# Kernel tuning notes

Measured on AMD Instinct MI355X. Metric: run time of the kernel, lower is better.

The kernel has to match this reference:

```python
import jax, jax.numpy as jnp
import numpy as np

B, S, D, H = 1, 2048, 1024, 16
HD = D // H  # head_dim = 64


def _split_heads(x):
    # [B,S,D] -> [B,H,S,HD]
    return x.reshape(B, S, H, HD).transpose(0, 2, 1, 3)


def setup_inputs() -> dict:
    key = jax.random.key(0)
    ks = jax.random.split(key, 8)
    p = 0.02
    return {
        "hidden_states": jax.random.normal(ks[0], (B, S, D), jnp.float32),
        "knowledge": jax.random.normal(ks[1], (B, S, D), jnp.float32),
        "Wq": jax.random.normal(ks[2], (2 * D, D), jnp.float32) * p,
        "Wk_know": jax.random.normal(ks[3], (D, D), jnp.float32) * p,
        "Wk_mlp": jax.random.normal(ks[4], (D, D), jnp.float32) * p,
        "Wv_know": jax.random.normal(ks[5], (D, D), jnp.float32) * p,
        "Wv_mlp": jax.random.normal(ks[6], (D, D), jnp.float32) * p,
        "Wo": jax.random.normal(ks[7], (D, D), jnp.float32) * p,
    }


def reference(hidden_states, knowledge, Wq, Wk_know, Wk_mlp, Wv_know, Wv_mlp, Wo):
    shared = jnp.concatenate([hidden_states, knowledge], axis=-1)  # [B,S,2D]
    q = _split_heads(shared @ Wq)            # [B,H,S,HD]
    k_know = _split_heads(knowledge @ Wk_know)
    k_mlp = _split_heads(hidden_states @ Wk_mlp)
    v_know = _split_heads(knowledge @ Wv_know)
    v_mlp = _split_heads(hidden_states @ Wv_mlp)

    scale = jnp.asarray(D, jnp.float32) ** 0.5  # note: full embed_dim, not head_dim
    mask_value = jnp.finfo(jnp.float32).min
    causal = jnp.tril(jnp.ones((S, S), dtype=bool))  # [S,S]

    s_know = jnp.einsum("bhqd,bhkd->bhqk", q, k_know) / scale
    s_know = jnp.where(causal, s_know, mask_value)
    s_mlp = jnp.einsum("bhqd,bhkd->bhqk", q, k_mlp) / scale
    s_mlp = jnp.where(causal, s_mlp, mask_value)

    concat_scores = jax.nn.softmax(jnp.concatenate([s_know, s_mlp], axis=-1), axis=-1)  # [B,H,S,2S]
    concat_values = jnp.concatenate([v_know, v_mlp], axis=-2)  # [B,H,2S,HD]
    out = jnp.einsum("bhqk,bhkd->bhqd", concat_scores, concat_values)
    out = out.transpose(0, 2, 1, 3).reshape(B, S, D) @ Wo  # merge heads + proj_o
    return out, concat_scores
```

## Files before the change

kernel.cpp:

```cpp
#include <hip/hip_runtime.h>

typedef unsigned short u16;
typedef float f32x4 __attribute__((ext_vector_type(4)));
typedef __bf16 bf16x8 __attribute__((ext_vector_type(8)));
typedef unsigned int u32x4 __attribute__((ext_vector_type(4)));
typedef u16 u16x4 __attribute__((ext_vector_type(4)));

#define S_ 2048
#define D_ 1024
#define H_ 16
#define HD_ 64

#define WAITV(N) asm volatile("s_waitcnt vmcnt(" #N ")" ::: "memory")
#define BAR() __builtin_amdgcn_s_barrier()
#define SFENCE() __builtin_amdgcn_sched_barrier(0)

__device__ __forceinline__ u16 f2bf(float f) {
  unsigned int u = __builtin_bit_cast(unsigned int, f);
  u += 0x7fffu + ((u >> 16) & 1u);
  return (u16)(u >> 16);
}

__device__ __forceinline__ f32x4 mfma16(bf16x8 a, bf16x8 b, f32x4 c) {
  return __builtin_amdgcn_mfma_f32_16x16x32_bf16(a, b, c, 0, 0, 0);
}

__device__ __forceinline__ float ex2(float x) {
  float r;
  asm("v_exp_f32 %0, %1\n\ts_nop 1" : "=v"(r) : "v"(x));
  return r;
}

__device__ __forceinline__ void gld_lds16(const u16* g, u16* l) {
  __builtin_amdgcn_global_load_lds((const __attribute__((address_space(1))) void*)g,
                                   (__attribute__((address_space(3))) void*)l, 16, 0, 0);
}

__global__ __launch_bounds__(256) void prep_kernel(
    const float* __restrict__ hs, const float* __restrict__ kn, const float* __restrict__ Wq,
    const float* __restrict__ Wkk, const float* __restrict__ Wvk, const float* __restrict__ Wkm,
    const float* __restrict__ Wvm, const float* __restrict__ Wo, u16* __restrict__ hs_bf,
    u16* __restrict__ kn_bf, u16* __restrict__ WqT, u16* __restrict__ WkvkT,
    u16* __restrict__ WkvmT, u16* __restrict__ WoT, int n4) {
  __shared__ float tile[32][33];
  int b = blockIdx.x;
  if (b < 4096) {
    int i = b * 256 + threadIdx.x;
    const float* s;
    u16* d;
    int j;
    if (i < n4) { s = hs; d = hs_bf; j = i; }
    else { j = i - n4; if (j >= n4) return; s = kn; d = kn_bf; }
    f32x4 v = *(const f32x4*)(s + (size_t)j * 4);
    u16x4 o;
    o[0] = f2bf(v[0]); o[1] = f2bf(v[1]); o[2] = f2bf(v[2]); o[3] = f2bf(v[3]);
    *(u16x4*)(d + (size_t)j * 4) = o;
    return;
  }
  int idx = b - 4096;
  int bc = idx & 31, y = idx >> 5;
  const float* W;
  u16* WT;
  int R, br;
  const size_t HM = (size_t)1024 * 1024;
  if (y < 64) { W = Wq; WT = WqT; R = 2048; br = y; }
  else {
    R = 1024; br = y & 31;
    switch ((y - 64) >> 5) {
      case 0: W = Wkk; WT = WkvkT; break;
      case 1: W = Wvk; WT = WkvkT + HM; break;
      case 2: W = Wkm; WT = WkvmT; break;
      case 3: W = Wvm; WT = WkvmT + HM; break;
      default: W = Wo; WT = WoT; break;
    }
  }
  int tx = threadIdx.x & 31, ty = threadIdx.x >> 5;
#pragma unroll
  for (int i = 0; i < 4; ++i)
    tile[ty + i * 8][tx] = W[(size_t)(br * 32 + ty + i * 8) * 1024 + bc * 32 + tx];
  __syncthreads();
#pragma unroll
  for (int i = 0; i < 4; ++i)
    WT[(size_t)(bc * 32 + ty + i * 8) * R + br * 32 + tx] = f2bf(tile[tx][ty + i * 8]);
}

template <int MODE, int MI, int NI>
__device__ __forceinline__ void gemm_body(u16* smem, const u16* A0, const u16* A1, int ksplit,
                                          const u16* BT, void* Cp, int K, int ldc, int bn,
                                          int bm) {
  constexpr int BM = MI * 32, BN = NI * 32;
  u16* const As0 = smem;
  u16* const Bs0 = smem + 2 * BM * 32;
  const int tid = threadIdx.x, l = tid & 63, w = tid >> 6;
  const int wm = w >> 1, wn = w & 1;
  f32x4 zf = {0.f, 0.f, 0.f, 0.f};
  f32x4 acc[MI][NI];
#pragma unroll
  for (int mi = 0; mi < MI; ++mi)
#pragma unroll
    for (int ni = 0; ni < NI; ++ni) acc[mi][ni] = zf;

  auto STAGE = [&](int b, int t) {
    int k0 = t * 32;
#pragma unroll
    for (int i = 0; i < MI / 2; ++i) {
      int idx = tid + i * 256, r = idx >> 2, c = idx & 3;
      int sc = c ^ ((r >> 1) & 3);
      int k = k0 + sc * 8;
      const u16* src = (k < ksplit) ? (A0 + (size_t)(bm * BM + r) * D_ + k)
                                    : (A1 + (size_t)(bm * BM + r) * D_ + (k - ksplit));
      gld_lds16(src, As0 + b * BM * 32 + idx * 8);
    }
#pragma unroll
    for (int i = 0; i < NI / 2; ++i) {
      int idx = tid + i * 256, r = idx >> 2, c = idx & 3;
      int sc = c ^ ((r >> 1) & 3);
      gld_lds16(BT + (size_t)(bn * BN + r) * K + k0 + sc * 8, Bs0 + b * BN * 32 + idx * 8);
    }
  };

  const int nt = K >> 5;
  STAGE(0, 0);
  int cur = 0;
  for (int t = 0; t < nt; ++t) {
    if (t + 1 < nt) {
      STAGE(cur ^ 1, t + 1);
      if constexpr (MI + NI == 8) { WAITV(4); } else { WAITV(3); }
    } else {
      WAITV(0);
    }
    BAR(); SFENCE();
    const u16* Asc = As0 + cur * BM * 32;
    const u16* Bsc = Bs0 + cur * BN * 32;
    bf16x8 af[MI], bfr[NI];
#pragma unroll
    for (int mi = 0; mi < MI; ++mi) {
      int row = wm * (MI * 16) + mi * 16 + (l & 15);
      int slot = (l >> 4) ^ ((row >> 1) & 3);
      af[mi] = __builtin_bit_cast(bf16x8, *(const u32x4*)(Asc + row * 32 + slot * 8));
    }
#pragma unroll
    for (int ni = 0; ni < NI; ++ni) {
      int row = wn * (NI * 16) + ni * 16 + (l & 15);
      int slot = (l >> 4) ^ ((row >> 1) & 3);
      bfr[ni] = __builtin_bit_cast(bf16x8, *(const u32x4*)(Bsc + row * 32 + slot * 8));
    }
#pragma unroll
    for (int mi = 0; mi < MI; ++mi)
#pragma unroll
      for (int ni = 0; ni < NI; ++ni) acc[mi][ni] = mfma16(af[mi], bfr[ni], acc[mi][ni]);
    SFENCE(); BAR();
    cur ^= 1;
  }

  if constexpr (MODE == 2) {
#pragma unroll
    for (int mi = 0; mi < MI; ++mi)
#pragma unroll
      for (int ni = 0; ni < NI; ++ni) {
        u16x4 pk;
#pragma unroll
        for (int r = 0; r < 4; ++r) pk[r] = f2bf(acc[mi][ni][r]);
        int n = bn * BN + wn * (NI * 16) + ni * 16 + (l & 15);
        int m0 = bm * BM + wm * (MI * 16) + mi * 16 + (l >> 4) * 4;
        *(u16x4*)((u16*)Cp + (size_t)n * S_ + m0) = pk;
      }
  } else if constexpr (MODE == 0) {
    __syncthreads();
    u16* Cs = smem;
#pragma unroll
    for (int mi = 0; mi < MI; ++mi)
#pragma unroll
      for (int ni = 0; ni < NI; ++ni)
#pragma unroll
        for (int r = 0; r < 4; ++r) {
          int row = wm * (MI * 16) + mi * 16 + (l >> 4) * 4 + r;
          int col = wn * (NI * 16) + ni * 16 + (l & 15);
          Cs[row * 144 + col] = f2bf(acc[mi][ni][r]);
        }
    __syncthreads();
    constexpr int CPR = BN / 8;
#pragma unroll
    for (int i = 0; i < BM * CPR / 256; ++i) {
      int idx = tid + i * 256;
      int lr = idx / CPR, cc = idx % CPR;
      u32x4 v = *(const u32x4*)(Cs + lr * 144 + cc * 8);
      *(u32x4*)((u16*)Cp + (size_t)(bm * BM + lr) * ldc + bn * BN + cc * 8) = v;
    }
  } else {
    __syncthreads();
    float* Cs = (float*)smem;
#pragma unroll
    for (int mi = 0; mi < MI; ++mi)
#pragma unroll
      for (int ni = 0; ni < NI; ++ni)
#pragma unroll
        for (int r = 0; r < 4; ++r) {
          int row = wm * (MI * 16) + mi * 16 + (l >> 4) * 4 + r;
          int col = wn * (NI * 16) + ni * 16 + (l & 15);
          Cs[row * 136 + col] = acc[mi][ni][r];
        }
    __syncthreads();
    constexpr int CPR = BN / 4;
#pragma unroll
    for (int i = 0; i < BM * CPR / 256; ++i) {
      int idx = tid + i * 256;
      int lr = idx / CPR, cc = idx % CPR;
      f32x4 v = *(const f32x4*)(Cs + lr * 136 + cc * 4);
      __builtin_nontemporal_store(v, (f32x4*)((float*)Cp + (size_t)(bm * BM + lr) * ldc +
                                              bn * BN + cc * 4));
    }
  }
}

__global__ __launch_bounds__(256) void proj_gemm(const u16* __restrict__ hs_bf,
                                                 const u16* __restrict__ kn_bf,
                                                 const u16* __restrict__ WqT,
                                                 const u16* __restrict__ WkvkT,
                                                 const u16* __restrict__ WkvmT,
                                                 u16* __restrict__ qb, u16* __restrict__ kk,
                                                 u16* __restrict__ km, u16* __restrict__ vkT,
                                                 u16* __restrict__ vmT) {
  __shared__ __attribute__((aligned(16))) u16 smem[18432];
  int bid = blockIdx.x;
  int xcd = bid & 7, ixd = bid >> 3;
  int bm, bn;
  if (ixd < 16) {
    bm = xcd * 2 + (ixd >> 3);
    bn = ixd & 7;
  } else if (ixd >= 64 && ixd < 80) {
    return;
  } else {
    int s = (ixd < 64) ? (ixd - 16) : (48 + (ixd - 80));
    bm = xcd * 2 + (s >> 5);
    bn = 8 + (s & 31);
  }
  const size_t HM = (size_t)1024 * 1024;
  const int BIG = 1 << 30;
  if (bn < 8) {
    gemm_body<0, 4, 4>(smem, hs_bf, kn_bf, 1024, WqT, qb, 2048, 1024, bn, bm);
  } else if (bn < 16) {
    gemm_body<0, 4, 4>(smem, kn_bf, kn_bf, BIG, WkvkT, kk, 1024, 1024, bn - 8, bm);
  } else if (bn < 24) {
    gemm_body<2, 4, 4>(smem, kn_bf, kn_bf, BIG, WkvkT + HM, vkT, 1024, 0, bn - 16, bm);
  } else if (bn < 32) {
    gemm_body<0, 4, 4>(smem, hs_bf, hs_bf, BIG, WkvmT, km, 1024, 1024, bn - 24, bm);
  } else {
    gemm_body<2, 4, 4>(smem, hs_bf, hs_bf, BIG, WkvmT + HM, vmT, 1024, 0, bn - 32, bm);
  }
}

__global__ __launch_bounds__(256) void out_gemm(const u16* __restrict__ aob,
                                                const u16* __restrict__ WoT,
                                                float* __restrict__ out) {
  __shared__ __attribute__((aligned(16))) u16 smem[17408];
  int bid = blockIdx.x;
  int xcd = bid & 7, i = bid >> 3;
  int bm = xcd * 4 + (i >> 3), bn = i & 7;
  gemm_body<1, 2, 4>(smem, aob, aob, 1 << 30, WoT, out, 1024, 1024, bn, bm);
}

__device__ __forceinline__ void stage_async64_t512(u16* dst, const u16* src, int stride,
                                                   int tid) {
  int ci = tid;
  int r = ci >> 3, c = ci & 7;
  int sc = c ^ (r & 7);
  gld_lds16(src + (size_t)r * stride + sc * 8, dst + ci * 8);
}

__device__ __forceinline__ bf16x8 ld_frag64(const u16* lds, int rowbase, int chunkbase, int l) {
  int row = rowbase + (l & 15);
  int chunk = chunkbase + (l >> 4);
  int slot = chunk ^ (row & 7);
  return __builtin_bit_cast(bf16x8, *(const u32x4*)(lds + row * 64 + slot * 8));
}

__global__ __launch_bounds__(512) void attn_kernel(const u16* __restrict__ qb,
                                                   const u16* __restrict__ kk,
                                                   const u16* __restrict__ km,
                                                   const u16* __restrict__ vkT,
                                                   const u16* __restrict__ vmT,
                                                   float* __restrict__ scores,
                                                   u16* __restrict__ ao) {
  const int fid = blockIdx.x;
  const int xcd = fid & 7, ixd = fid >> 3;
  const int h = xcd * 2 + (ixd >> 5);
  const int j = ixd & 31;
  const int a = j >> 1;
  const int qt = (((j & 1) ^ (ixd >> 5)) == 0) ? (31 - a) : a;
  const int tid = threadIdx.x, w = tid >> 6, l = tid & 63;
  const int wk = w & 3, kh = w >> 2;
  const int nt = qt + 1;
  const int NT = 2 * nt;
  const int qrow0 = qt * 64;
  const int q16 = l & 15, c4 = l >> 4;
  const int qme = qrow0 + wk * 16 + q16;
  const float sc2 = 0.04508422f;

  __shared__ u16 qs[64 * 64];
  __shared__ u16 kv4[4][64 * 64];
  __shared__ u16 ps[64 * 64];
  __shared__ float stat[128];

  auto kptr = [&](int it) {
    int hf = it >= nt;
    int t = it - (hf ? nt : 0);
    const u16* kb = hf ? km : kk;
    return kb + (size_t)(t * 64) * 1024 + h * HD_;
  };
  auto vptr = [&](int it) {
    int hf = it >= nt;
    int t = it - (hf ? nt : 0);
    const u16* vb = hf ? vmT : vkT;
    return vb + (size_t)(h * HD_) * S_ + t * 64;
  };

  {
    int r = tid >> 3, c = tid & 7;
    u32x4 v = *(const u32x4*)(qb + (size_t)(qrow0 + r) * D_ + h * HD_ + c * 8);
    *(u32x4*)(qs + r * 64 + ((c ^ (r & 7)) * 8)) = v;
  }
  __syncthreads();
  bf16x8 qA0 = ld_frag64(qs, wk * 16, 0, l);
  bf16x8 qA1 = ld_frag64(qs, wk * 16, 4, l);

  float aa[4] = {0.f, 0.f, 0.f, 0.f};
  stage_async64_t512(kv4[0], kptr(0), 1024, tid);
  stage_async64_t512(kv4[1], kptr(1), 1024, tid);
  for (int p = 0; p < NT; p += 2) {
    WAITV(0);
    BAR(); SFENCE();
    int base = ((p >> 1) & 1) ? 2 : 0;
    if (p + 2 < NT) {
      int nb = base ^ 2;
      stage_async64_t512(kv4[nb], kptr(p + 2), 1024, tid);
      stage_async64_t512(kv4[nb + 1], kptr(p + 3), 1024, tid);
    }
    __builtin_amdgcn_s_setprio(1);
#pragma unroll
    for (int half = 0; half < 2; ++half) {
      int it = p + half;
      const u16* ksb = kv4[base + half];
      int domask = (it == nt - 1) || (it == NT - 1);
      int tbase = (it - (it >= nt ? nt : 0)) * 64;
      f32x4 zfv = {0.f, 0.f, 0.f, 0.f};
#pragma unroll
      for (int jf = 0; jf < 2; ++jf) {
        int kf = kh * 2 + jf;
        f32x4 z = zfv;
        z = mfma16(ld_frag64(ksb, kf * 16, 0, l), qA0, z);
        z = mfma16(ld_frag64(ksb, kf * 16, 4, l), qA1, z);
#pragma unroll
        for (int r = 0; r < 4; ++r) {
          float v = z[r];
          if (domask) {
            int key = tbase + kf * 16 + c4 * 4 + r;
            if (key > qme) v = -1e30f;
          }
          aa[r] += ex2(v * sc2);
        }
      }
    }
    __builtin_amdgcn_s_setprio(0);
    SFENCE();
  }
  float psum = (aa[0] + aa[1]) + (aa[2] + aa[3]);
  psum += __shfl_xor(psum, 16, 64);
  psum += __shfl_xor(psum, 32, 64);
  if (l < 16) stat[w * 16 + l] = psum;
  __syncthreads();
  const float lsum = stat[wk * 16 + q16] + stat[(wk + 4) * 16 + q16];
  const float moff = __log2f(lsum);

  f32x4 zf = {0.f, 0.f, 0.f, 0.f};
  f32x4 o[4];
#pragma unroll
  for (int df = 0; df < 4; ++df) o[df] = zf;

  float* const srow0 = scores + ((size_t)h * S_ + qme) * (2 * S_) + c4 * 4;
  const int prow = wk * 16 + q16;
  const int swz8 = (q16 & 7) << 1;

  stage_async64_t512(kv4[0], kptr(0), 1024, tid);
  stage_async64_t512(kv4[2], vptr(0), S_, tid);
  int cur = 0;
  for (int it = 0; it < NT; ++it) {
    if (it == 0) { WAITV(0); } else { WAITV(2); }
    BAR(); SFENCE();
    if (it + 1 < NT) {
      stage_async64_t512(kv4[cur ^ 1], kptr(it + 1), 1024, tid);
      stage_async64_t512(kv4[2 + (cur ^ 1)], vptr(it + 1), S_, tid);
    }
    int domask = (it == nt - 1) || (it == NT - 1);
    int hf = it >= nt;
    int tbase = (it - (hf ? nt : 0)) * 64;
    float pv[8];
    __builtin_amdgcn_s_setprio(1);
#pragma unroll
    for (int jf = 0; jf < 2; ++jf) {
      int kf = kh * 2 + jf;
      f32x4 z = zf;
      z = mfma16(ld_frag64(kv4[cur], kf * 16, 0, l), qA0, z);
      z = mfma16(ld_frag64(kv4[cur], kf * 16, 4, l), qA1, z);
#pragma unroll
      for (int r = 0; r < 4; ++r) {
        float v = z[r];
        if (domask) {
          int key = tbase + kf * 16 + c4 * 4 + r;
          if (key > qme) v = -1e30f;
        }
        pv[jf * 4 + r] = ex2(__builtin_fmaf(v, sc2, -moff));
      }
    }
    __builtin_amdgcn_s_setprio(0);
    float* srow = srow0 + hf * S_ + tbase;
#pragma unroll
    for (int jf = 0; jf < 2; ++jf) {
      int kf = kh * 2 + jf;
      f32x4 s4 = {pv[jf * 4], pv[jf * 4 + 1], pv[jf * 4 + 2], pv[jf * 4 + 3]};
      *(f32x4*)(srow + kf * 16) = s4;
    }
#pragma unroll
    for (int jf = 0; jf < 2; ++jf) {
      int kf = kh * 2 + jf;
      u16x4 pk;
#pragma unroll
      for (int r = 0; r < 4; ++r) pk[r] = f2bf(pv[jf * 4 + r]);
      int slot8 = (kf * 4 + c4) ^ swz8;
      *(u16x4*)(ps + prow * 64 + slot8 * 4) = pk;
    }
    __builtin_amdgcn_s_setprio(1);
    {
      bf16x8 pa = ld_frag64(ps, wk * 16, kh * 4, l);
#pragma unroll
      for (int df = 0; df < 4; ++df)
        o[df] = mfma16(ld_frag64(kv4[2 + cur], df * 16, kh * 4, l), pa, o[df]);
    }
    __builtin_amdgcn_s_setprio(0);
    SFENCE();
    cur ^= 1;
  }

  __syncthreads();
  float* obuf = (float*)kv4;
  if (kh == 1) {
#pragma unroll
    for (int df = 0; df < 4; ++df)
#pragma unroll
      for (int r = 0; r < 4; ++r)
        obuf[((wk * 4 + df) * 16 + c4 * 4 + r) * 16 + q16] = o[df][r];
  }
  __syncthreads();
  if (kh == 0) {
#pragma unroll
    for (int df = 0; df < 4; ++df) {
      u16x4 pk;
#pragma unroll
      for (int r = 0; r < 4; ++r) {
        float t = o[df][r] + obuf[((wk * 4 + df) * 16 + c4 * 4 + r) * 16 + q16];
        pk[r] = f2bf(t);
      }
      *(u16x4*)(ao + (size_t)qme * D_ + h * HD_ + df * 16 + c4 * 4) = pk;
    }
  }

  int zc = 2048 - nt * 64;
  if (zc > 0) {
    int vph = zc >> 2;
    f32x4 zero = {0.f, 0.f, 0.f, 0.f};
    float* base = scores + ((size_t)h * S_ + qrow0) * (2 * S_) + nt * 64;
    for (int row = 0; row < 64; ++row) {
      float* rp = base + (size_t)row * (2 * S_);
      for (int i = tid; i < vph; i += 512)
        __builtin_nontemporal_store(zero, (f32x4*)(rp + i * 4));
      for (int i = tid; i < vph; i += 512)
        __builtin_nontemporal_store(zero, (f32x4*)(rp + S_ + i * 4));
    }
  }
}

extern "C" void kernel_launch(void* const* d_in, const int* in_sizes, int n_in, void* d_out,
                              int out_size, void* d_ws, size_t ws_size, hipStream_t stream) {
  const float* hs = (const float*)d_in[0];
  const float* kn = (const float*)d_in[1];
  const float* Wq = (const float*)d_in[2];
  const float* Wkk = (const float*)d_in[3];
  const float* Wkm = (const float*)d_in[4];
  const float* Wvk = (const float*)d_in[5];
  const float* Wvm = (const float*)d_in[6];
  const float* Wo = (const float*)d_in[7];
  float* out = (float*)d_out;
  float* scores = out + (size_t)S_ * D_;

  const size_t M2 = (size_t)S_ * D_;
  u16* ws = (u16*)d_ws;
  u16* hs_bf = ws;
  u16* kn_bf = hs_bf + M2;
  u16* WqT = kn_bf + M2;
  u16* WkvkT = WqT + M2;
  u16* WkvmT = WkvkT + M2;
  u16* WoT = WkvmT + M2;
  u16* qb = WoT + M2 / 2;
  u16* kk = qb + M2;
  u16* km = kk + M2;
  u16* vkT = km + M2;
  u16* vmT = vkT + M2;
  u16* aob = vmT + M2;

  int n4 = (int)(M2 / 4);
  prep_kernel<<<11264, 256, 0, stream>>>(hs, kn, Wq, Wkk, Wvk, Wkm, Wvm, Wo, hs_bf, kn_bf, WqT,
                                         WkvkT, WkvmT, WoT, n4);
  proj_gemm<<<768, 256, 0, stream>>>(hs_bf, kn_bf, WqT, WkvkT, WkvmT, qb, kk, km, vkT, vmT);
  attn_kernel<<<512, 512, 0, stream>>>(qb, kk, km, vkT, vmT, scores, aob);
  out_gemm<<<256, 256, 0, stream>>>(aob, WoT, out);
}
```

Measured before the change: 191.3 us.

## Process two KV tiles per barrier with 4-deep K/V rings; retile output GEMM

The attention kernel's second pass (PV) now uses separate 4-slot ring buffers for K and V. It prefetches two tiles at a time and computes two tiles per barrier, which halves the number of block-wide synchronisations and deepens the prefetch. The Q staging buffer is folded into the P scratch buffer to save LDS, though total LDS per block still grows to about 72KB. The output projection GEMM switches to a narrower N tile with twice as many blocks, and the GEMM wait count gains a case for that tile shape. The cost is more LDS per block and more in-flight loads.

New measurement: 180.6 us (median of 2 runs). -5.6%, faster.

```diff
diff --git a/kernel.cpp b/kernel.cpp
--- a/kernel.cpp
+++ b/kernel.cpp
@@ -125,7 +125,9 @@
   for (int t = 0; t < nt; ++t) {
     if (t + 1 < nt) {
       STAGE(cur ^ 1, t + 1);
-      if constexpr (MI + NI == 8) { WAITV(4); } else { WAITV(3); }
+      if constexpr (MI + NI == 8) { WAITV(4); }
+      else if constexpr (MI + NI == 6) { WAITV(3); }
+      else { WAITV(2); }
     } else {
       WAITV(0);
     }
@@ -256,8 +258,8 @@
   __shared__ __attribute__((aligned(16))) u16 smem[17408];
   int bid = blockIdx.x;
   int xcd = bid & 7, i = bid >> 3;
-  int bm = xcd * 4 + (i >> 3), bn = i & 7;
-  gemm_body<1, 2, 4>(smem, aob, aob, 1 << 30, WoT, out, 1024, 1024, bn, bm);
+  int bm = xcd * 4 + (i >> 4), bn = i & 15;
+  gemm_body<1, 2, 2>(smem, aob, aob, 1 << 30, WoT, out, 1024, 1024, bn, bm);
 }
 
 __device__ __forceinline__ void stage_async64_t512(u16* dst, const u16* src, int stride,
@@ -297,8 +299,8 @@
   const int qme = qrow0 + wk * 16 + q16;
   const float sc2 = 0.04508422f;
 
-  __shared__ u16 qs[64 * 64];
-  __shared__ u16 kv4[4][64 * 64];
+  __shared__ u16 kr[4][64 * 64];
+  __shared__ u16 vr[4][64 * 64];
   __shared__ u16 ps[64 * 64];
   __shared__ float stat[128];
 
@@ -318,29 +320,28 @@
   {
     int r = tid >> 3, c = tid & 7;
     u32x4 v = *(const u32x4*)(qb + (size_t)(qrow0 + r) * D_ + h * HD_ + c * 8);
-    *(u32x4*)(qs + r * 64 + ((c ^ (r & 7)) * 8)) = v;
+    *(u32x4*)(ps + r * 64 + ((c ^ (r & 7)) * 8)) = v;
   }
   __syncthreads();
-  bf16x8 qA0 = ld_frag64(qs, wk * 16, 0, l);
-  bf16x8 qA1 = ld_frag64(qs, wk * 16, 4, l);
+  bf16x8 qA0 = ld_frag64(ps, wk * 16, 0, l);
+  bf16x8 qA1 = ld_frag64(ps, wk * 16, 4, l);
+  __syncthreads();
 
   float aa[4] = {0.f, 0.f, 0.f, 0.f};
-  stage_async64_t512(kv4[0], kptr(0), 1024, tid);
-  stage_async64_t512(kv4[1], kptr(1), 1024, tid);
+  stage_async64_t512(kr[0], kptr(0), 1024, tid);
+  stage_async64_t512(kr[1], kptr(1), 1024, tid);
   for (int p = 0; p < NT; p += 2) {
     WAITV(0);
     BAR(); SFENCE();
-    int base = ((p >> 1) & 1) ? 2 : 0;
     if (p + 2 < NT) {
-      int nb = base ^ 2;
-      stage_async64_t512(kv4[nb], kptr(p + 2), 1024, tid);
-      stage_async64_t512(kv4[nb + 1], kptr(p + 3), 1024, tid);
+      stage_async64_t512(kr[(p + 2) & 3], kptr(p + 2), 1024, tid);
+      stage_async64_t512(kr[(p + 3) & 3], kptr(p + 3), 1024, tid);
     }
     __builtin_amdgcn_s_setprio(1);
 #pragma unroll
     for (int half = 0; half < 2; ++half) {
       int it = p + half;
-      const u16* ksb = kv4[base + half];
+      const u16* ksb = kr[it & 3];
       int domask = (it == nt - 1) || (it == NT - 1);
       int tbase = (it - (it >= nt ? nt : 0)) * 64;
       f32x4 zfv = {0.f, 0.f, 0.f, 0.f};
@@ -381,68 +382,74 @@
   const int prow = wk * 16 + q16;
   const int swz8 = (q16 & 7) << 1;
 
-  stage_async64_t512(kv4[0], kptr(0), 1024, tid);
-  stage_async64_t512(kv4[2], vptr(0), S_, tid);
-  int cur = 0;
-  for (int it = 0; it < NT; ++it) {
-    if (it == 0) { WAITV(0); } else { WAITV(2); }
+  stage_async64_t512(kr[0], kptr(0), 1024, tid);
+  stage_async64_t512(kr[1], kptr(1), 1024, tid);
+  stage_async64_t512(vr[0], vptr(0), S_, tid);
+  stage_async64_t512(vr[1], vptr(1), S_, tid);
+  for (int p = 0; p < NT; p += 2) {
+    if (p == 0) { WAITV(0); } else { WAITV(4); }
     BAR(); SFENCE();
-    if (it + 1 < NT) {
-      stage_async64_t512(kv4[cur ^ 1], kptr(it + 1), 1024, tid);
-      stage_async64_t512(kv4[2 + (cur ^ 1)], vptr(it + 1), S_, tid);
-    }
-    int domask = (it == nt - 1) || (it == NT - 1);
-    int hf = it >= nt;
-    int tbase = (it - (hf ? nt : 0)) * 64;
-    float pv[8];
-    __builtin_amdgcn_s_setprio(1);
-#pragma unroll
-    for (int jf = 0; jf < 2; ++jf) {
-      int kf = kh * 2 + jf;
-      f32x4 z = zf;
-      z = mfma16(ld_frag64(kv4[cur], kf * 16, 0, l), qA0, z);
-      z = mfma16(ld_frag64(kv4[cur], kf * 16, 4, l), qA1, z);
-#pragma unroll
-      for (int r = 0; r < 4; ++r) {
-        float v = z[r];
-        if (domask) {
-          int key = tbase + kf * 16 + c4 * 4 + r;
-          if (key > qme) v = -1e30f;
+    if (p + 2 < NT) {
+      stage_async64_t512(kr[(p + 2) & 3], kptr(p + 2), 1024, tid);
+      stage_async64_t512(kr[(p + 3) & 3], kptr(p + 3), 1024, tid);
+      stage_async64_t512(vr[(p + 2) & 3], vptr(p + 2), S_, tid);
+      stage_async64_t512(vr[(p + 3) & 3], vptr(p + 3), S_, tid);
+    }
+#pragma unroll
+    for (int half = 0; half < 2; ++half) {
+      int it = p + half;
+      int domask = (it == nt - 1) || (it == NT - 1);
+      int hf = it >= nt;
+      int tbase = (it - (hf ? nt : 0)) * 64;
+      float pv[8];
+      __builtin_amdgcn_s_setprio(1);
+#pragma unroll
+      for (int jf = 0; jf < 2; ++jf) {
+        int kf = kh * 2 + jf;
+        f32x4 z = zf;
+        z = mfma16(ld_frag64(kr[it & 3], kf * 16, 0, l), qA0, z);
+        z = mfma16(ld_frag64(kr[it & 3], kf * 16, 4, l), qA1, z);
+#pragma unroll
+        for (int r = 0; r < 4; ++r) {
+          float v = z[r];
+          if (domask) {
+            int key = tbase + kf * 16 + c4 * 4 + r;
+            if (key > qme) v = -1e30f;
+          }
+          pv[jf * 4 + r] = ex2(__builtin_fmaf(v, sc2, -moff));
         }
-        pv[jf * 4 + r] = ex2(__builtin_fmaf(v, sc2, -moff));
-      }
-    }
-    __builtin_amdgcn_s_setprio(0);
-    float* srow = srow0 + hf * S_ + tbase;
-#pragma unroll
-    for (int jf = 0; jf < 2; ++jf) {
-      int kf = kh * 2 + jf;
-      f32x4 s4 = {pv[jf * 4], pv[jf * 4 + 1], pv[jf * 4 + 2], pv[jf * 4 + 3]};
-      *(f32x4*)(srow + kf * 16) = s4;
-    }
-#pragma unroll
-    for (int jf = 0; jf < 2; ++jf) {
-      int kf = kh * 2 + jf;
-      u16x4 pk;
-#pragma unroll
-      for (int r = 0; r < 4; ++r) pk[r] = f2bf(pv[jf * 4 + r]);
-      int slot8 = (kf * 4 + c4) ^ swz8;
-      *(u16x4*)(ps + prow * 64 + slot8 * 4) = pk;
-    }
-    __builtin_amdgcn_s_setprio(1);
-    {
-      bf16x8 pa = ld_frag64(ps, wk * 16, kh * 4, l);
-#pragma unroll
-      for (int df = 0; df < 4; ++df)
-        o[df] = mfma16(ld_frag64(kv4[2 + cur], df * 16, kh * 4, l), pa, o[df]);
-    }
-    __builtin_amdgcn_s_setprio(0);
+      }
+      __builtin_amdgcn_s_setprio(0);
+      float* srow = srow0 + hf * S_ + tbase;
+#pragma unroll
+      for (int jf = 0; jf < 2; ++jf) {
+        int kf = kh * 2 + jf;
+        f32x4 s4 = {pv[jf * 4], pv[jf * 4 + 1], pv[jf * 4 + 2], pv[jf * 4 + 3]};
+        *(f32x4*)(srow + kf * 16) = s4;
+      }
+#pragma unroll
+      for (int jf = 0; jf < 2; ++jf) {
+        int kf = kh * 2 + jf;
+        u16x4 pk;
+#pragma unroll
+        for (int r = 0; r < 4; ++r) pk[r] = f2bf(pv[jf * 4 + r]);
+        int slot8 = (kf * 4 + c4) ^ swz8;
+        *(u16x4*)(ps + prow * 64 + slot8 * 4) = pk;
+      }
+      __builtin_amdgcn_s_setprio(1);
+      {
+        bf16x8 pa = ld_frag64(ps, wk * 16, kh * 4, l);
+#pragma unroll
+        for (int df = 0; df < 4; ++df)
+          o[df] = mfma16(ld_frag64(vr[it & 3], df * 16, kh * 4, l), pa, o[df]);
+      }
+      __builtin_amdgcn_s_setprio(0);
+    }
     SFENCE();
-    cur ^= 1;
   }
 
   __syncthreads();
-  float* obuf = (float*)kv4;
+  float* obuf = (float*)kr;
   if (kh == 1) {
 #pragma unroll
     for (int df = 0; df < 4; ++df)
@@ -512,5 +519,5 @@
                                          WkvkT, WkvmT, WoT, n4);
   proj_gemm<<<768, 256, 0, stream>>>(hs_bf, kn_bf, WqT, WkvkT, WkvmT, qb, kk, km, vkT, vmT);
   attn_kernel<<<512, 512, 0, stream>>>(qb, kk, km, vkT, vmT, scores, aob);
-  out_gemm<<<256, 256, 0, stream>>>(aob, WoT, out);
-}
+  out_gemm<<<512, 256, 0, stream>>>(aob, WoT, out);
+}
```
